# Optimization experiments

Measured on AMD Instinct MI355X. Metric: run time of the kernel, lower is better.

## Reference

```python
import jax, jax.numpy as jnp
import numpy as np


def setup_inputs() -> dict:
    key = jax.random.key(0)
    k1, k2 = jax.random.split(key)
    N, C, H, W = 1, 32, 128, 240
    return {
        "left_feature": jax.random.normal(k1, (N, C, H, W), dtype=jnp.float32),
        "right_feature": jax.random.normal(k2, (N, C, H, W), dtype=jnp.float32),
        "max_disparity": 192,
    }


def reference(left_feature, right_feature, max_disparity):
    # left_feature, right_feature: (N, C, H, W)
    N, C, H, W = left_feature.shape
    D4 = max_disparity // 4
    i_idx = jnp.arange(D4)[:, None]          # (D4, 1) disparity index
    w_idx = jnp.arange(W)[None, :]           # (1, W)  column index
    valid = (w_idx >= i_idx)                 # (D4, W): cols written at disparity i
    m = valid[None, None, :, None, :]        # (1, 1, D4, 1, W)

    # Left half: cost[:, :C, i, :, i:] = left[:, :, :, i:] (unshifted, masked)
    left_vol = jnp.where(m, left_feature[:, :, None, :, :], jnp.zeros((), left_feature.dtype))

    # Right half: cost[:, C:, i, :, i:] = right[:, :, :, :-i] -> right shifted by i
    shift = jnp.clip(w_idx - i_idx, 0, W - 1)              # (D4, W)
    right_sh = right_feature[:, :, :, shift]               # (N, C, H, D4, W)
    right_vol = jnp.where(m, jnp.transpose(right_sh, (0, 1, 3, 2, 4)),
                          jnp.zeros((), right_feature.dtype))

    # (N, 2C, D4, H, W)
    return jnp.concatenate([left_vol, right_vol], axis=1)
```

## Files before the change

kernel.cpp:

```cpp
#include <hip/hip_runtime.h>


constexpr int C      = 32;
constexpr int H      = 128;
constexpr int W      = 240;
constexpr int D4     = 48;
constexpr int W4     = W / 4;
constexpr int SLICE4 = H * W4;
constexpr int BLOCK  = 256;
constexpr int ITERS  = SLICE4 / BLOCK;

typedef float f32x4 __attribute__((ext_vector_type(4)));

__global__ void __launch_bounds__(256) cost_volume_kernel(
    const float* __restrict__ left,
    const float* __restrict__ right,
    float* __restrict__ out) {
    const int slice = blockIdx.x;
    const int d     = slice % D4;
    const int c2    = slice / D4;
    const bool is_left = (c2 < C);

    f32x4* __restrict__ out4 =
        reinterpret_cast<f32x4*>(out) + (long)slice * SLICE4;
    const int tid = threadIdx.x;

    if (is_left) {
        const f32x4* __restrict__ src4 =
            reinterpret_cast<const f32x4*>(left + c2 * H * W);
#pragma unroll 6
        for (int it = 0; it < ITERS; ++it) {
            const int flat = it * BLOCK + tid;
            const int w0   = (flat % W4) * 4;
            f32x4 v = src4[flat];
            if (w0 < d) {
#pragma unroll
                for (int j = 0; j < 4; ++j)
                    if (w0 + j < d) v[j] = 0.0f;
            }
            __builtin_nontemporal_store(v, out4 + flat);
        }
    } else {
        const float* __restrict__ src = right + (c2 - C) * H * W;
#pragma unroll 6
        for (int it = 0; it < ITERS; ++it) {
            const int flat = it * BLOCK + tid;
            const int h    = flat / W4;
            const int w0   = (flat % W4) * 4;
            const float* __restrict__ row = src + h * W - d;
            f32x4 v;
#pragma unroll
            for (int j = 0; j < 4; ++j) {
                const int wj = w0 + j;
                v[j] = (wj >= d) ? row[wj] : 0.0f;
            }
            __builtin_nontemporal_store(v, out4 + flat);
        }
    }
}

extern "C" void kernel_launch(void* const* d_in, const int* in_sizes, int n_in,
                              void* d_out, int out_size, void* d_ws,
                              size_t ws_size, hipStream_t stream) {
    const float* left  = (const float*)d_in[0];
    const float* right = (const float*)d_in[1];
    float* out = (float*)d_out;

    const int grid = 2 * C * D4;
    cost_volume_kernel<<<grid, BLOCK, 0, stream>>>(left, right, out);
}
```

Measured before the change: 89.61 us.

## Tile by row chunk and reuse loaded inputs across all disparities

Each block now handles 8 rows of one channel and loops over all 48 disparities. Input rows are loaded once, into registers for the left half or into padded LDS for the right half, and reused for every disparity instead of being re-read from global/L2 per slice. This cuts read traffic roughly 48x, leaving the kernel bound by output writes. In exchange it adds LDS bank-conflict padding, a __syncthreads, and uneven thread utilisation, since 480 vec4s are spread over 512 threads.

```diff
diff --git a/kernel.cpp b/kernel.cpp
--- a/kernel.cpp
+++ b/kernel.cpp
@@ -1,60 +1,84 @@
 #include <hip/hip_runtime.h>
 
 
-constexpr int C      = 32;
-constexpr int H      = 128;
-constexpr int W      = 240;
-constexpr int D4     = 48;
-constexpr int W4     = W / 4;
-constexpr int SLICE4 = H * W4;
-constexpr int BLOCK  = 256;
-constexpr int ITERS  = SLICE4 / BLOCK;
+constexpr int C   = 32;
+constexpr int H   = 128;
+constexpr int W   = 240;
+constexpr int D4  = 48;
+constexpr int W4  = W / 4;
+constexpr int RPB = 8;
+constexpr int HC  = H / RPB;
+constexpr int CH4 = RPB * W4;
+constexpr int BLOCK = 256;
+constexpr int PAD_OFF = 48;
 
 typedef float f32x4 __attribute__((ext_vector_type(4)));
+
+__device__ __forceinline__ int pidx(int x) { return x + (x >> 5); }
 
 __global__ void __launch_bounds__(256) cost_volume_kernel(
     const float* __restrict__ left,
     const float* __restrict__ right,
     float* __restrict__ out) {
-    const int slice = blockIdx.x;
-    const int d     = slice % D4;
-    const int c2    = slice / D4;
+    __shared__ float rowbuf[2080];
+
+    const int blk = blockIdx.x;
+    const int hc  = blk % HC;
+    const int c2  = blk / HC;
+    const int h0  = hc * RPB;
+    const int tid = threadIdx.x;
     const bool is_left = (c2 < C);
 
-    f32x4* __restrict__ out4 =
-        reinterpret_cast<f32x4*>(out) + (long)slice * SLICE4;
-    const int tid = threadIdx.x;
+    f32x4* __restrict__ outb = reinterpret_cast<f32x4*>(out)
+        + ((long)(c2 * D4) * H + h0) * W4;
+    const long dstride = (long)H * W4;
+
+    const int f0  = tid;
+    const int f1  = tid + BLOCK;
+    const bool has1 = (f1 < CH4);
+    const int f1c = has1 ? f1 : (CH4 - 1);
+    const int w0_0 = (f0 % W4) * 4;
+    const int w0_1 = (f1c % W4) * 4;
 
     if (is_left) {
         const f32x4* __restrict__ src4 =
-            reinterpret_cast<const f32x4*>(left + c2 * H * W);
-#pragma unroll 6
-        for (int it = 0; it < ITERS; ++it) {
-            const int flat = it * BLOCK + tid;
-            const int w0   = (flat % W4) * 4;
-            f32x4 v = src4[flat];
-            if (w0 < d) {
+            reinterpret_cast<const f32x4*>(left + (c2 * H + h0) * W);
+        const f32x4 t0 = src4[f0];
+        const f32x4 t1 = has1 ? src4[f1] : f32x4{0.f, 0.f, 0.f, 0.f};
+#pragma unroll 4
+        for (int d = 0; d < D4; ++d) {
+            f32x4 v0, v1;
 #pragma unroll
-                for (int j = 0; j < 4; ++j)
-                    if (w0 + j < d) v[j] = 0.0f;
+            for (int j = 0; j < 4; ++j) {
+                v0[j] = (w0_0 + j >= d) ? t0[j] : 0.0f;
+                v1[j] = (w0_1 + j >= d) ? t1[j] : 0.0f;
             }
-            __builtin_nontemporal_store(v, out4 + flat);
+            f32x4* __restrict__ o = outb + d * dstride;
+            __builtin_nontemporal_store(v0, o + f0);
+            if (has1) __builtin_nontemporal_store(v1, o + f1);
         }
     } else {
-        const float* __restrict__ src = right + (c2 - C) * H * W;
-#pragma unroll 6
-        for (int it = 0; it < ITERS; ++it) {
-            const int flat = it * BLOCK + tid;
-            const int h    = flat / W4;
-            const int w0   = (flat % W4) * 4;
-            const float* __restrict__ row = src + h * W - d;
-            f32x4 v;
+        const float* __restrict__ src = right + ((c2 - C) * H + h0) * W;
+        for (int f = tid; f < CH4; f += BLOCK) {
+            f32x4 t = reinterpret_cast<const f32x4*>(src)[f];
+            const int base = PAD_OFF + f * 4;
+#pragma unroll
+            for (int j = 0; j < 4; ++j) rowbuf[pidx(base + j)] = t[j];
+        }
+        __syncthreads();
+        const int b0 = PAD_OFF + (f0  / W4) * W + w0_0;
+        const int b1 = PAD_OFF + (f1c / W4) * W + w0_1;
+#pragma unroll 4
+        for (int d = 0; d < D4; ++d) {
+            f32x4 v0, v1;
 #pragma unroll
             for (int j = 0; j < 4; ++j) {
-                const int wj = w0 + j;
-                v[j] = (wj >= d) ? row[wj] : 0.0f;
+                v0[j] = (w0_0 + j >= d) ? rowbuf[pidx(b0 - d + j)] : 0.0f;
+                v1[j] = (w0_1 + j >= d) ? rowbuf[pidx(b1 - d + j)] : 0.0f;
             }
-            __builtin_nontemporal_store(v, out4 + flat);
+            f32x4* __restrict__ o = outb + d * dstride;
+            __builtin_nontemporal_store(v0, o + f0);
+            if (has1) __builtin_nontemporal_store(v1, o + f1);
         }
     }
 }
@@ -66,6 +90,6 @@
     const float* right = (const float*)d_in[1];
     float* out = (float*)d_out;
 
-    const int grid = 2 * C * D4;
+    const int grid = 2 * C * HC;
     cost_volume_kernel<<<grid, BLOCK, 0, stream>>>(left, right, out);
 }
```

Result: faster. 78.70 us (-12.2%).
